# Kernel optimization log

Measured on AMD Instinct MI355X. Metric: run time of the kernel, lower is better.

The kernel has to match this reference:

```python
import math
import jax, jax.numpy as jnp
import numpy as np

B, LQ, LK = 4, 1024, 1024
D_MODEL, NHEAD, FFN = 1024, 16, 4096
DEPTH = D_MODEL // NHEAD  # 64
MAX_REL = 1024
EPS = 1e-5


def _rel_embedding():
    # fixed (non-learned) buffer: clamped relative-position indices used as float values
    length = max(MAX_REL, DEPTH)
    r = np.arange(length)
    mat = np.clip(r[None, :] - r[:, None], -MAX_REL, MAX_REL) + MAX_REL
    return jnp.asarray(mat[:MAX_REL, :DEPTH], jnp.float32)  # [MAX_REL, DEPTH]


def _skew(rel, length_k):
    # rel: [B, H, Lq, Lq] -> relative logits aligned to key positions [B, H, Lq, Lk]
    b, h, lq, m = rel.shape
    assert lq == m
    rel = jnp.pad(rel, ((0, 0), (0, 0), (0, 0), (1, 0)))
    rel = rel.reshape(b, h, lq + 1, lq)[:, :, 1:, :]
    if length_k > lq:
        rel = jnp.pad(rel, ((0, 0), (0, 0), (0, 0), (0, length_k - lq)))
    elif length_k < lq:
        rel = rel[:, :, :, :length_k]
    return rel


def _split_heads(t):
    b, l, _ = t.shape
    return t.reshape(b, l, NHEAD, DEPTH).transpose(0, 2, 1, 3)  # [b,h,l,d]


def _rga(x_q, x_kv, Wq, bq, Wo, bo, mask, rel_e):
    # NOTE: faithful to source - Q, K and V all use query_projection
    q = _split_heads(x_q @ Wq + bq)
    k = _split_heads(x_kv @ Wq + bq)
    v = _split_heads(x_kv @ Wq + bq)
    lq, lk = q.shape[2], k.shape[2]
    logits = jnp.einsum('bhqd,bhkd->bhqk', q, k)
    start = max(0, MAX_REL - lq)
    ke = rel_e[start:, :]  # [min(MAX_REL,lq), DEPTH]
    rel = jnp.einsum('bhld,md->bhlm', q, ke)
    logits = (logits + _skew(rel, lk)) / math.sqrt(DEPTH)
    if mask is not None:
        logits = jnp.where(mask, logits, jnp.asarray(-1e9, logits.dtype))
    w = jax.nn.softmax(logits, axis=-1)
    out = jnp.einsum('bhqk,bhkd->bhqd', w, v)
    out = out.transpose(0, 2, 1, 3).reshape(x_q.shape[0], lq, D_MODEL)
    return out @ Wo + bo


def _layernorm(x, g, b):
    mu = jnp.mean(x, axis=-1, keepdims=True)
    var = jnp.mean(jnp.square(x - mu), axis=-1, keepdims=True)
    return (x - mu) * jax.lax.rsqrt(var + EPS) * g + b


def setup_inputs() -> dict:
    key = jax.random.key(0)
    ks = jax.random.split(key, 12)
    s = 0.02
    inp = {
        'tgt': jax.random.normal(ks[0], (B, LQ, D_MODEL), jnp.float32),
        'memory': jax.random.normal(ks[1], (B, LK, D_MODEL), jnp.float32),
        'tgt_mask': jnp.tril(jnp.ones((LQ, LQ), dtype=bool)),
        'sa_Wq': jax.random.normal(ks[2], (D_MODEL, D_MODEL), jnp.float32) * s,
        'sa_bq': jnp.zeros((D_MODEL,), jnp.float32),
        'sa_Wo': jax.random.normal(ks[3], (D_MODEL, D_MODEL), jnp.float32) * s,
        'sa_bo': jnp.zeros((D_MODEL,), jnp.float32),
        'ca_Wq': jax.random.normal(ks[4], (D_MODEL, D_MODEL), jnp.float32) * s,
        'ca_bq': jnp.zeros((D_MODEL,), jnp.float32),
        'ca_Wo': jax.random.normal(ks[5], (D_MODEL, D_MODEL), jnp.float32) * s,
        'ca_bo': jnp.zeros((D_MODEL,), jnp.float32),
        'ffn_W1': jax.random.normal(ks[6], (D_MODEL, FFN), jnp.float32) * s,
        'ffn_b1': jnp.zeros((FFN,), jnp.float32),
        'ffn_W2': jax.random.normal(ks[7], (FFN, D_MODEL), jnp.float32) * s,
        'ffn_b2': jnp.zeros((D_MODEL,), jnp.float32),
        'ln1_g': jnp.ones((D_MODEL,), jnp.float32), 'ln1_b': jnp.zeros((D_MODEL,), jnp.float32),
        'ln2_g': jnp.ones((D_MODEL,), jnp.float32), 'ln2_b': jnp.zeros((D_MODEL,), jnp.float32),
        'ln3_g': jnp.ones((D_MODEL,), jnp.float32), 'ln3_b': jnp.zeros((D_MODEL,), jnp.float32),
    }
    return inp


def reference(tgt, memory, tgt_mask, sa_Wq, sa_bq, sa_Wo, sa_bo, ca_Wq, ca_bq, ca_Wo, ca_bo,
              ffn_W1, ffn_b1, ffn_W2, ffn_b2, ln1_g, ln1_b, ln2_g, ln2_b, ln3_g, ln3_b):
    rel_e = _rel_embedding()
    # self-attention (relative-global) with causal mask
    x = tgt + _rga(tgt, tgt, sa_Wq, sa_bq, sa_Wo, sa_bo, tgt_mask, rel_e)
    x = _layernorm(x, ln1_g, ln1_b)
    # cross-attention (also relative-global per source)
    x = x + _rga(x, memory, ca_Wq, ca_bq, ca_Wo, ca_bo, None, rel_e)
    x = _layernorm(x, ln2_g, ln2_b)
    # FFN
    h = jax.nn.relu(x @ ffn_W1 + ffn_b1)
    x = x + (h @ ffn_W2 + ffn_b2)
    x = _layernorm(x, ln3_g, ln3_b)
    return x
```

## Files before the change

### kernel.cpp

```cpp
#include <hip/hip_runtime.h>

typedef __attribute__((ext_vector_type(4))) float f32x4;
typedef __attribute__((ext_vector_type(8))) short s16x8;
typedef __attribute__((ext_vector_type(4))) unsigned short u16x4;

__device__ __forceinline__ unsigned short f2bf(float x) {
  union { float f; unsigned u; } un; un.f = x;
  unsigned u = un.u;
  u += 0x7FFFu + ((u >> 16) & 1u);
  return (unsigned short)(u >> 16);
}
__device__ __forceinline__ float bf2f(unsigned short h) {
  union { unsigned u; float f; } un; un.u = ((unsigned)h) << 16; return un.f;
}

__device__ __forceinline__ f32x4 mfma16(s16x8 a, s16x8 b, f32x4 c) {
  asm("v_mfma_f32_16x16x32_bf16 %0, %1, %2, %0" : "+v"(c) : "v"(a), "v"(b));
  return c;
}

__device__ __forceinline__ void gld16(const void* g, void* l) {
  __builtin_amdgcn_global_load_lds(
      (const __attribute__((address_space(1))) void*)g,
      (__attribute__((address_space(3))) void*)l, 16, 0, 0);
}

template<bool RELU, bool RESID, bool OUT_BF16>
__global__ __launch_bounds__(256, 2) void bgemm_k(
    const unsigned short* __restrict__ Ab, const unsigned short* __restrict__ Bb,
    const float* __restrict__ bias, const float* __restrict__ resid,
    void* __restrict__ Cp, int M, int N, int K, int lbx)
{
  __shared__ __align__(16) unsigned short As[2][128 * 64];
  __shared__ __align__(16) unsigned short Bs[2][128 * 64];

  const int nwg = gridDim.x;
  const int bid = blockIdx.x;
  const int swz = (bid & 7) * (nwg >> 3) + (bid >> 3);
  const int nbx_m1 = (1 << lbx) - 1;
  const int n0 = (swz & nbx_m1) * 128;
  const int m0 = (swz >> lbx) * 128;

  const int tid = threadIdx.x;
  const int lane = tid & 63;
  const int w = tid >> 6;
  const int wm = w >> 1, wn = w & 1;
  const int li = lane & 15, g = lane >> 4;

  f32x4 acc[4][4] = {};

#define STAGE(buf, kt) do { \
    const int k0_ = (kt) * 64; \
    _Pragma("unroll") \
    for (int i_ = 0; i_ < 4; i_++) { \
      int lin = i_ * 256 + tid; int row = lin >> 3; \
      int cg = (lin & 7) ^ (row & 7); \
      gld16(Ab + (size_t)(m0 + row) * K + k0_ + cg * 8, &As[buf][lin * 8]); \
    } \
    _Pragma("unroll") \
    for (int i_ = 0; i_ < 4; i_++) { \
      int lin = i_ * 256 + tid; int row = lin >> 3; \
      int cg = (lin & 7) ^ (row & 7); \
      gld16(Bb + (size_t)(n0 + row) * K + k0_ + cg * 8, &Bs[buf][lin * 8]); \
    } \
  } while (0)

  const int NT = K >> 6;
  STAGE(0, 0);
  for (int t = 0; t < NT; ++t) {
    const int cur = t & 1;
    if (t + 1 < NT) {
      STAGE(cur ^ 1, t + 1);
      asm volatile("s_waitcnt vmcnt(8)" ::: "memory");
    } else {
      asm volatile("s_waitcnt vmcnt(0)" ::: "memory");
    }
    __builtin_amdgcn_sched_barrier(0);
    __builtin_amdgcn_s_barrier();
    __builtin_amdgcn_sched_barrier(0);
#pragma unroll
    for (int ks = 0; ks < 2; ++ks) {
      s16x8 af[4], bf[4];
#pragma unroll
      for (int mt = 0; mt < 4; mt++) {
        int row = wm * 64 + mt * 16 + li;
        int slot = (4 * ks + g) ^ (row & 7);
        af[mt] = *(const s16x8*)&As[cur][row * 64 + slot * 8];
      }
#pragma unroll
      for (int nt = 0; nt < 4; nt++) {
        int row = wn * 64 + nt * 16 + li;
        int slot = (4 * ks + g) ^ (row & 7);
        bf[nt] = *(const s16x8*)&Bs[cur][row * 64 + slot * 8];
      }
#pragma unroll
      for (int mt = 0; mt < 4; mt++)
#pragma unroll
        for (int nt = 0; nt < 4; nt++)
          acc[mt][nt] = mfma16(af[mt], bf[nt], acc[mt][nt]);
    }
    __builtin_amdgcn_sched_barrier(0);
    __builtin_amdgcn_s_barrier();
    __builtin_amdgcn_sched_barrier(0);
  }
#undef STAGE

  asm volatile("s_nop 7\n\ts_nop 7" :::);
#pragma unroll
  for (int mt = 0; mt < 4; mt++) {
    int mrow = m0 + wm * 64 + mt * 16 + 4 * g;
#pragma unroll
    for (int nt = 0; nt < 4; nt++) {
      int ncol = n0 + wn * 64 + nt * 16 + li;
      float bv = bias ? bias[ncol] : 0.f;
#pragma unroll
      for (int r = 0; r < 4; r++) {
        int mr = mrow + r;
        float v = acc[mt][nt][r] + bv;
        if (RESID) v += resid[(size_t)mr * N + ncol];
        if (RELU) v = fmaxf(v, 0.f);
        if (OUT_BF16) ((unsigned short*)Cp)[(size_t)mr * N + ncol] = f2bf(v);
        else          ((float*)Cp)[(size_t)mr * N + ncol] = v;
      }
    }
  }
}

__global__ __launch_bounds__(256, 2) void bgemm_pk(
    const unsigned short* __restrict__ Ab, const unsigned short* __restrict__ Bb,
    float* __restrict__ P0, float* __restrict__ P1,
    int M, int N, int K, int KH, int lbx)
{
  __shared__ __align__(16) unsigned short As[2][128 * 64];
  __shared__ __align__(16) unsigned short Bs[2][128 * 64];

  const int nwg = gridDim.x;
  const int bid = blockIdx.x;
  const int swz = (bid & 7) * (nwg >> 3) + (bid >> 3);
  const int nbx_m1 = (1 << lbx) - 1;
  const int n0 = (swz & nbx_m1) * 128;
  int m0 = (swz >> lbx) * 128;

  int kb = 0;
  float* Pp = P0;
  if (m0 >= M) { m0 -= M; kb = KH; Pp = P1; }

  const int tid = threadIdx.x;
  const int lane = tid & 63;
  const int w = tid >> 6;
  const int wm = w >> 1, wn = w & 1;
  const int li = lane & 15, g = lane >> 4;

  f32x4 acc[4][4] = {};

#define PSTAGE(buf, kt) do { \
    const int k0_ = kb + (kt) * 64; \
    _Pragma("unroll") \
    for (int i_ = 0; i_ < 4; i_++) { \
      int lin = i_ * 256 + tid; int row = lin >> 3; \
      int cg = (lin & 7) ^ (row & 7); \
      gld16(Ab + (size_t)(m0 + row) * K + k0_ + cg * 8, &As[buf][lin * 8]); \
    } \
    _Pragma("unroll") \
    for (int i_ = 0; i_ < 4; i_++) { \
      int lin = i_ * 256 + tid; int row = lin >> 3; \
      int cg = (lin & 7) ^ (row & 7); \
      gld16(Bb + (size_t)(n0 + row) * K + k0_ + cg * 8, &Bs[buf][lin * 8]); \
    } \
  } while (0)

  const int NT = KH >> 6;
  PSTAGE(0, 0);
  for (int t = 0; t < NT; ++t) {
    const int cur = t & 1;
    if (t + 1 < NT) {
      PSTAGE(cur ^ 1, t + 1);
      asm volatile("s_waitcnt vmcnt(8)" ::: "memory");
    } else {
      asm volatile("s_waitcnt vmcnt(0)" ::: "memory");
    }
    __builtin_amdgcn_sched_barrier(0);
    __builtin_amdgcn_s_barrier();
    __builtin_amdgcn_sched_barrier(0);
#pragma unroll
    for (int ks = 0; ks < 2; ++ks) {
      s16x8 af[4], bf[4];
#pragma unroll
      for (int mt = 0; mt < 4; mt++) {
        int row = wm * 64 + mt * 16 + li;
        int slot = (4 * ks + g) ^ (row & 7);
        af[mt] = *(const s16x8*)&As[cur][row * 64 + slot * 8];
      }
#pragma unroll
      for (int nt = 0; nt < 4; nt++) {
        int row = wn * 64 + nt * 16 + li;
        int slot = (4 * ks + g) ^ (row & 7);
        bf[nt] = *(const s16x8*)&Bs[cur][row * 64 + slot * 8];
      }
#pragma unroll
      for (int mt = 0; mt < 4; mt++)
#pragma unroll
        for (int nt = 0; nt < 4; nt++)
          acc[mt][nt] = mfma16(af[mt], bf[nt], acc[mt][nt]);
    }
    __builtin_amdgcn_sched_barrier(0);
    __builtin_amdgcn_s_barrier();
    __builtin_amdgcn_sched_barrier(0);
  }
#undef PSTAGE

  asm volatile("s_nop 7\n\ts_nop 7" :::);
#pragma unroll
  for (int mt = 0; mt < 4; mt++) {
    int mrow = m0 + wm * 64 + mt * 16 + 4 * g;
#pragma unroll
    for (int nt = 0; nt < 4; nt++) {
      int ncol = n0 + wn * 64 + nt * 16 + li;
#pragma unroll
      for (int r = 0; r < 4; r++) {
        int mr = mrow + r;
        Pp[(size_t)mr * N + ncol] = acc[mt][nt][r];
      }
    }
  }
}

__global__ __launch_bounds__(256, 2) void sgemm_k(
    const unsigned short* __restrict__ Ah, const unsigned short* __restrict__ Al,
    const unsigned short* __restrict__ A2h, const unsigned short* __restrict__ A2l,
    const unsigned short* __restrict__ Bh, const unsigned short* __restrict__ Bl,
    const float* __restrict__ bias,
    unsigned short* __restrict__ Cb, unsigned short* __restrict__ C2b,
    int Ms, int M, int N, int K, int lbx)
{
  __shared__ __align__(16) unsigned short AsH[128 * 64];
  __shared__ __align__(16) unsigned short AsL[128 * 64];
  __shared__ __align__(16) unsigned short BsH[128 * 64];
  __shared__ __align__(16) unsigned short BsL[128 * 64];

  const int nwg = gridDim.x;
  const int bid = blockIdx.x;
  const int swz = (bid & 7) * (nwg >> 3) + (bid >> 3);
  const int nbx_m1 = (1 << lbx) - 1;
  const int n0 = (swz & nbx_m1) * 128;
  int m0 = (swz >> lbx) * 128;

  const unsigned short* Ahp = Ah;
  const unsigned short* Alp = Al;
  unsigned short* Cp = Cb;
  if (m0 >= Ms) { Ahp = A2h; Alp = A2l; Cp = C2b; m0 -= Ms; }

  const int tid = threadIdx.x;
  const int lane = tid & 63;
  const int w = tid >> 6;
  const int wm = w >> 1, wn = w & 1;
  const int li = lane & 15, g = lane >> 4;

  f32x4 acc[4][4] = {};

  const int NT = K >> 6;
  for (int t = 0; t < NT; ++t) {
    __syncthreads();
#pragma unroll
    for (int i = 0; i < 4; i++) {
      int lin = i * 256 + tid; int row = lin >> 3;
      int cg = (lin & 7) ^ (row & 7);
      size_t offA = (size_t)(m0 + row) * K + t * 64 + cg * 8;
      size_t offB = (size_t)(n0 + row) * K + t * 64 + cg * 8;
      gld16(Ahp + offA, &AsH[lin * 8]);
      gld16(Alp + offA, &AsL[lin * 8]);
      gld16(Bh + offB, &BsH[lin * 8]);
      gld16(Bl + offB, &BsL[lin * 8]);
    }
    asm volatile("s_waitcnt vmcnt(0)" ::: "memory");
    __syncthreads();
#pragma unroll
    for (int ks = 0; ks < 2; ++ks) {
      s16x8 ah[4], al[4], bh[4], bl[4];
#pragma unroll
      for (int mt = 0; mt < 4; mt++) {
        int row = wm * 64 + mt * 16 + li;
        int slot = (4 * ks + g) ^ (row & 7);
        ah[mt] = *(const s16x8*)&AsH[row * 64 + slot * 8];
        al[mt] = *(const s16x8*)&AsL[row * 64 + slot * 8];
      }
#pragma unroll
      for (int nt = 0; nt < 4; nt++) {
        int row = wn * 64 + nt * 16 + li;
        int slot = (4 * ks + g) ^ (row & 7);
        bh[nt] = *(const s16x8*)&BsH[row * 64 + slot * 8];
        bl[nt] = *(const s16x8*)&BsL[row * 64 + slot * 8];
      }
#pragma unroll
      for (int mt = 0; mt < 4; mt++)
#pragma unroll
        for (int nt = 0; nt < 4; nt++) {
          acc[mt][nt] = mfma16(ah[mt], bh[nt], acc[mt][nt]);
          acc[mt][nt] = mfma16(ah[mt], bl[nt], acc[mt][nt]);
          acc[mt][nt] = mfma16(al[mt], bh[nt], acc[mt][nt]);
        }
    }
  }

  asm volatile("s_nop 7\n\ts_nop 7" :::);
#pragma unroll
  for (int mt = 0; mt < 4; mt++) {
    int mrow = m0 + wm * 64 + mt * 16 + 4 * g;
#pragma unroll
    for (int nt = 0; nt < 4; nt++) {
      int ncol = n0 + wn * 64 + nt * 16 + li;
      float bv = bias[ncol];
#pragma unroll
      for (int r = 0; r < 4; r++) {
        int mr = mrow + r;
        Cp[(size_t)mr * N + ncol] = f2bf(acc[mt][nt][r] + bv);
      }
    }
  }
}

__device__ __forceinline__ void dev_tc(const float* __restrict__ W,
    unsigned short* __restrict__ WT, int K, int N, int bid, char* ldsu)
{
  unsigned short (*Ls)[65] = (unsigned short (*)[65])ldsu;
  int ntx = N >> 6;
  int ty = bid / ntx, tx = bid - ty * ntx;
  int r0 = ty << 6, c0 = tx << 6;
  int tid = threadIdx.x;
  int rl = tid >> 4, cl = (tid & 15) << 2;
#pragma unroll
  for (int rr = 0; rr < 4; rr++) {
    f32x4 v = *(const f32x4*)&W[(size_t)(r0 + rl + rr * 16) * N + c0 + cl];
#pragma unroll
    for (int j = 0; j < 4; j++) Ls[rl + rr * 16][cl + j] = f2bf(v[j]);
  }
  __syncthreads();
#pragma unroll
  for (int rr = 0; rr < 4; rr++) {
    int nl = rl + rr * 16;
    u16x4 o;
#pragma unroll
    for (int j = 0; j < 4; j++) o[j] = Ls[cl + j][nl];
    *(u16x4*)&WT[(size_t)(c0 + nl) * K + r0 + cl] = o;
  }
}

__device__ __forceinline__ void dev_tc2(const float* __restrict__ W,
    unsigned short* __restrict__ WTh, unsigned short* __restrict__ WTl,
    int K, int N, int bid, char* ldsu)
{
  float (*Ls)[65] = (float (*)[65])ldsu;
  int ntx = N >> 6;
  int ty = bid / ntx, tx = bid - ty * ntx;
  int r0 = ty << 6, c0 = tx << 6;
  int tid = threadIdx.x;
  int rl = tid >> 4, cl = (tid & 15) << 2;
#pragma unroll
  for (int rr = 0; rr < 4; rr++) {
    f32x4 v = *(const f32x4*)&W[(size_t)(r0 + rl + rr * 16) * N + c0 + cl];
#pragma unroll
    for (int j = 0; j < 4; j++) Ls[rl + rr * 16][cl + j] = v[j];
  }
  __syncthreads();
#pragma unroll
  for (int rr = 0; rr < 4; rr++) {
    int nl = rl + rr * 16;
    u16x4 oh, ol;
#pragma unroll
    for (int j = 0; j < 4; j++) {
      float v = Ls[cl + j][nl];
      unsigned short h = f2bf(v);
      oh[j] = h; ol[j] = f2bf(v - bf2f(h));
    }
    *(u16x4*)&WTh[(size_t)(c0 + nl) * K + r0 + cl] = oh;
    *(u16x4*)&WTl[(size_t)(c0 + nl) * K + r0 + cl] = ol;
  }
}

__global__ __launch_bounds__(256) void prep_w_k(
    const float* saWq, const float* caWq, const float* saWo, const float* caWo,
    const float* W1, const float* W2,
    unsigned short* WqTsaH, unsigned short* WqTsaL,
    unsigned short* WqTcaH, unsigned short* WqTcaL,
    unsigned short* WoTsa, unsigned short* WoTca,
    unsigned short* W1T, unsigned short* W2T)
{
  __shared__ __align__(16) char LDSU[64 * 65 * 4];
  int bid = blockIdx.x;
  if (bid < 256)       dev_tc2(saWq, WqTsaH, WqTsaL, 1024, 1024, bid, LDSU);
  else if (bid < 512)  dev_tc2(caWq, WqTcaH, WqTcaL, 1024, 1024, bid - 256, LDSU);
  else if (bid < 768)  dev_tc (saWo, WoTsa, 1024, 1024, bid - 512, LDSU);
  else if (bid < 1024) dev_tc (caWo, WoTca, 1024, 1024, bid - 768, LDSU);
  else if (bid < 2048) dev_tc (W1, W1T, 1024, 4096, bid - 1024, LDSU);
  else                 dev_tc (W2, W2T, 4096, 1024, bid - 2048, LDSU);
}

__device__ __forceinline__ void dev_cvt2row(const float* __restrict__ X,
    unsigned short* __restrict__ H, unsigned short* __restrict__ L, int bid)
{
  int i = (bid * 256 + threadIdx.x) * 4;
  f32x4 v = *(const f32x4*)&X[i];
  u16x4 hh, ll;
#pragma unroll
  for (int j = 0; j < 4; j++) {
    unsigned short h = f2bf(v[j]);
    hh[j] = h; ll[j] = f2bf(v[j] - bf2f(h));
  }
  *(u16x4*)&H[i] = hh;
  *(u16x4*)&L[i] = ll;
}

__device__ __forceinline__ void dev_wrel(const float* __restrict__ Wq,
    float* __restrict__ Wr, int bid)
{
  int idx = bid * 256 + threadIdx.x;
  int k = idx >> 4, h = idx & 15;
  const float* src = Wq + (size_t)k * 1024 + h * 64;
  float a = 0.f, s = 0.f;
#pragma unroll
  for (int d = 0; d < 64; d += 4) {
    f32x4 v = *(const f32x4*)&src[d];
#pragma unroll
    for (int j = 0; j < 4; j++) { a += v[j] * (float)(d + j + 1024); s += v[j]; }
  }
  Wr[k * 32 + h] = a;
  Wr[k * 32 + 16 + h] = s;
}

__device__ __forceinline__ void dev_crel(const float* __restrict__ bq,
    float* __restrict__ cr)
{
  int h = threadIdx.x;
  if (h < 16) {
    float a = 0.f, s = 0.f;
    for (int d = 0; d < 64; d++) { float v = bq[h * 64 + d]; a += v * (float)(d + 1024); s += v; }
    cr[h] = a; cr[16 + h] = s;
  }
}

__global__ __launch_bounds__(256) void prep_a_k(
    const float* tgt, const float* mem,
    unsigned short* tgth, unsigned short* tgtl,
    unsigned short* memh, unsigned short* meml,
    const float* saWq, const float* caWq, float* wrelsa, float* wrelca,
    const float* sabq, const float* cabq, float* crelsa, float* crelca)
{
  int bid = blockIdx.x;
  if (bid < 4096)       dev_cvt2row(tgt, tgth, tgtl, bid);
  else if (bid < 8192)  dev_cvt2row(mem, memh, meml, bid - 4096);
  else if (bid < 8256)  dev_wrel(saWq, wrelsa, bid - 8192);
  else if (bid < 8320)  dev_wrel(caWq, wrelca, bid - 8256);
  else if (bid == 8320) dev_crel(sabq, crelsa);
  else                  dev_crel(cabq, crelca);
}

__global__ __launch_bounds__(256) void relgemm_k(const float* __restrict__ X,
    const float* __restrict__ Wr, const float* __restrict__ cr,
    float* __restrict__ Out)
{
  __shared__ float Xs[8][256];
  __shared__ float Ws[256][32];
  int r0 = blockIdx.x * 8;
  int tid = threadIdx.x;
  int rl = tid >> 5, col = tid & 31;
  float acc = 0.f;
  for (int kc = 0; kc < 1024; kc += 256) {
    __syncthreads();
    {
      const float* xs = X + (size_t)(r0 + rl) * 1024 + kc + col * 8;
      *(f32x4*)&Xs[rl][col * 8] = *(const f32x4*)xs;
      *(f32x4*)&Xs[rl][col * 8 + 4] = *(const f32x4*)(xs + 4);
    }
    {
      const float* wsrc = Wr + (size_t)(kc + tid) * 32;
#pragma unroll
      for (int i = 0; i < 8; i++) *(f32x4*)&Ws[tid][i * 4] = *(const f32x4*)&wsrc[i * 4];
    }
    __syncthreads();
#pragma unroll 8
    for (int kk = 0; kk < 256; ++kk) acc += Xs[rl][kk] * Ws[kk][col];
  }
  Out[(size_t)(r0 + rl) * 32 + col] = acc + cr[col];
}

template<bool CAUSAL>
__global__ __launch_bounds__(512) void attn_k(
    const unsigned short* __restrict__ Qb, const unsigned short* __restrict__ KVb,
    const float* __restrict__ rAS, unsigned short* __restrict__ Ob)
{
  const int bh = blockIdx.x;
  const int b = bh >> 4, h = bh & 15;
  const int y = blockIdx.y;
  const int tid = threadIdx.x, lane = tid & 63, w = tid >> 6;
  const int g = lane >> 4, li = lane & 15;

  __shared__ __align__(16) unsigned short Kt[64 * 64];
  __shared__ __align__(16) unsigned short KT[64 * 64];
  __shared__ __align__(16) unsigned short Pl[8][16 * 64];

  const int tile = CAUSAL ? ((w < 4) ? y : (15 - y)) : (2 * y + (w >> 2));
  const int q0 = tile * 64 + (w & 3) * 16;
  const int nkb = CAUSAL ? (16 - y) : 16;

  s16x8 qf[2];
  {
    const unsigned short* qrow = Qb + (size_t)(b * 1024 + q0 + li) * 1024 + h * 64;
    qf[0] = *(const s16x8*)&qrow[8 * g];
    qf[1] = *(const s16x8*)&qrow[8 * g + 32];
  }
  const float SCL2 = 0.125f * 1.44269504f;
  int qri[4];
  float C0c[4], C1c[4], rSc[4], rS1c[4];
#pragma unroll
  for (int r = 0; r < 4; r++) {
    int qr = q0 + 4 * g + r;
    qri[r] = qr;
    float rA = rAS[(size_t)(b * 1024 + qr) * 32 + h];
    float rS = rAS[(size_t)(b * 1024 + qr) * 32 + 16 + h];
    int q1 = (qr + 1 < 1024) ? qr + 1 : 1023;
    float rA1 = rAS[(size_t)(b * 1024 + q1) * 32 + h];
    float rS1 = rAS[(size_t)(b * 1024 + q1) * 32 + 16 + h];
    C0c[r]  = (rA + (float)(qr - 1023) * rS) * SCL2;
    rSc[r]  = rS * SCL2;
    C1c[r]  = (rA1 + (float)(qr + 2) * rS1) * SCL2;
    rS1c[r] = rS1 * SCL2;
  }

  float mrow[4], lrow[4];
#pragma unroll
  for (int r = 0; r < 4; r++) { mrow[r] = -3.0e38f; lrow[r] = 0.f; }
  f32x4 accO[4] = {};

  for (int kbk = 0; kbk < nkb; kbk++) {
    __syncthreads();
    {
      const unsigned short* src = KVb + (size_t)(b * 1024 + kbk * 64 + lane) * 1024 + h * 64 + w * 8;
      s16x8 v = *(const s16x8*)src;
      int slot = w ^ (lane & 7);
      *(s16x8*)&Kt[lane * 64 + slot * 8] = v;
#pragma unroll
      for (int j = 0; j < 8; j++) {
        int d = w * 8 + j;
        KT[d * 64 + (((lane >> 3) ^ (d & 7)) * 8) + (lane & 7)] = (unsigned short)v[j];
      }
    }
    __syncthreads();
    if (!CAUSAL || kbk <= tile) {
      const bool diag = CAUSAL && (kbk == tile);
      f32x4 accS[4];
#pragma unroll
      for (int nt = 0; nt < 4; nt++) {
        int krow = li + 16 * nt;
        f32x4 c = {};
#pragma unroll
        for (int ks = 0; ks < 2; ks++) {
          int slot = (g + 4 * ks) ^ (krow & 7);
          s16x8 kf = *(const s16x8*)&Kt[krow * 64 + slot * 8];
          c = mfma16(qf[ks], kf, c);
        }
        accS[nt] = c;
      }
      float pv[4][4];
      float bm[4];
#pragma unroll
      for (int r = 0; r < 4; r++) bm[r] = -3.0e38f;
#pragma unroll
      for (int nt = 0; nt < 4; nt++) {
        int kk = kbk * 64 + 16 * nt + li;
        float kkf = (float)kk;
#pragma unroll
        for (int r = 0; r < 4; r++) {
          float sk = (kk <= qri[r]) ? fmaf(kkf, -rSc[r], C0c[r])
                   : ((kk == qri[r] + 1) ? 0.f : fmaf(kkf, -rS1c[r], C1c[r]));
          float lg = fmaf(accS[nt][r], SCL2, sk);
          if (diag && kk > qri[r]) lg = -1.0e9f;
          pv[nt][r] = lg;
          bm[r] = fmaxf(bm[r], lg);
        }
      }
#pragma unroll
      for (int off = 1; off < 16; off <<= 1)
#pragma unroll
        for (int r = 0; r < 4; r++)
          bm[r] = fmaxf(bm[r], __shfl_xor(bm[r], off, 64));
      float scl[4], rsum[4];
#pragma unroll
      for (int r = 0; r < 4; r++) {
        float mnew = fmaxf(mrow[r], bm[r]);
        scl[r] = exp2f(mrow[r] - mnew);
        mrow[r] = mnew;
        rsum[r] = 0.f;
      }
#pragma unroll
      for (int nt = 0; nt < 4; nt++)
#pragma unroll
        for (int r = 0; r < 4; r++) {
          float p = exp2f(pv[nt][r] - mrow[r]);
          pv[nt][r] = p;
          rsum[r] += p;
        }
#pragma unroll
      for (int off = 1; off < 16; off <<= 1)
#pragma unroll
        for (int r = 0; r < 4; r++)
          rsum[r] += __shfl_xor(rsum[r], off, 64);
#pragma unroll
      for (int r = 0; r < 4; r++) lrow[r] = lrow[r] * scl[r] + rsum[r];
#pragma unroll
      for (int nt = 0; nt < 4; nt++)
#pragma unroll
        for (int r = 0; r < 4; r++) {
          int qq = 4 * g + r;
          int kkk = 16 * nt + li;
          int slot = (kkk >> 3) ^ (qq & 7);
          Pl[w][qq * 64 + slot * 8 + (kkk & 7)] = f2bf(pv[nt][r]);
        }
#pragma unroll
      for (int dt = 0; dt < 4; dt++)
#pragma unroll
        for (int r = 0; r < 4; r++) accO[dt][r] *= scl[r];
      s16x8 pfk[2];
#pragma unroll
      for (int ks = 0; ks < 2; ks++) {
        int slotA = (g + 4 * ks) ^ (li & 7);
        pfk[ks] = *(const s16x8*)&Pl[w][li * 64 + slotA * 8];
      }
#pragma unroll
      for (int dt = 0; dt < 4; dt++) {
#pragma unroll
        for (int ks = 0; ks < 2; ks++) {
          int drow = li + 16 * dt;
          int slotB = (g + 4 * ks) ^ (drow & 7);
          s16x8 vf = *(const s16x8*)&KT[drow * 64 + slotB * 8];
          accO[dt] = mfma16(pfk[ks], vf, accO[dt]);
        }
      }
    }
  }
  asm volatile("s_nop 7\n\ts_nop 7" :::);
#pragma unroll
  for (int dt = 0; dt < 4; dt++) {
    int dcol = h * 64 + li + 16 * dt;
#pragma unroll
    for (int r = 0; r < 4; r++) {
      int q = q0 + 4 * g + r;
      Ob[(size_t)(b * 1024 + q) * 1024 + dcol] = f2bf(accO[dt][r] / lrow[r]);
    }
  }
}

__global__ __launch_bounds__(256) void redln_k(
    const float* __restrict__ P0, const float* __restrict__ P1,
    const float* __restrict__ bias, const float* __restrict__ resid,
    const float* __restrict__ gw, const float* __restrict__ bw,
    float* __restrict__ O, unsigned short* __restrict__ Obh,
    unsigned short* __restrict__ Obl)
{
  int row = blockIdx.x;
  int tid = threadIdx.x;
  size_t base = (size_t)row * 1024 + tid * 4;
  f32x4 a = *(const f32x4*)&P0[base];
  f32x4 b = *(const f32x4*)&P1[base];
  f32x4 c = *(const f32x4*)&resid[base];
  f32x4 bv = *(const f32x4*)&bias[tid * 4];
  f32x4 v;
#pragma unroll
  for (int j = 0; j < 4; j++) v[j] = a[j] + b[j] + bv[j] + c[j];
  float s = v[0] + v[1] + v[2] + v[3];
  float s2 = v[0]*v[0] + v[1]*v[1] + v[2]*v[2] + v[3]*v[3];
#pragma unroll
  for (int off = 32; off > 0; off >>= 1) {
    s += __shfl_down(s, off, 64);
    s2 += __shfl_down(s2, off, 64);
  }
  __shared__ float rb[8];
  if ((tid & 63) == 0) { rb[tid >> 6] = s; rb[4 + (tid >> 6)] = s2; }
  __syncthreads();
  float S = rb[0] + rb[1] + rb[2] + rb[3];
  float S2 = rb[4] + rb[5] + rb[6] + rb[7];
  float mu = S * (1.f / 1024.f);
  float var = S2 * (1.f / 1024.f) - mu * mu;
  float rstd = rsqrtf(var + 1e-5f);
  f32x4 go = *(const f32x4*)&gw[tid * 4];
  f32x4 bo = *(const f32x4*)&bw[tid * 4];
  f32x4 r;
#pragma unroll
  for (int j = 0; j < 4; j++) r[j] = (v[j] - mu) * rstd * go[j] + bo[j];
  *(f32x4*)&O[base] = r;
  if (Obh) {
    u16x4 oh;
#pragma unroll
    for (int j = 0; j < 4; j++) oh[j] = f2bf(r[j]);
    *(u16x4*)&Obh[base] = oh;
    if (Obl) {
      u16x4 ol;
#pragma unroll
      for (int j = 0; j < 4; j++) ol[j] = f2bf(r[j] - bf2f(f2bf(r[j])));
      *(u16x4*)&Obl[base] = ol;
    }
  }
}

extern "C" void kernel_launch(void* const* d_in, const int* in_sizes, int n_in,
                              void* d_out, int out_size, void* d_ws, size_t ws_size,
                              hipStream_t stream)
{
  const float* tgt  = (const float*)d_in[0];
  const float* mem  = (const float*)d_in[1];
  const float* saWq = (const float*)d_in[3];
  const float* sabq = (const float*)d_in[4];
  const float* saWo = (const float*)d_in[5];
  const float* sabo = (const float*)d_in[6];
  const float* caWq = (const float*)d_in[7];
  const float* cabq = (const float*)d_in[8];
  const float* caWo = (const float*)d_in[9];
  const float* cabo = (const float*)d_in[10];
  const float* W1   = (const float*)d_in[11];
  const float* b1   = (const float*)d_in[12];
  const float* W2   = (const float*)d_in[13];
  const float* b2   = (const float*)d_in[14];
  const float* g1   = (const float*)d_in[15];
  const float* be1  = (const float*)d_in[16];
  const float* g2   = (const float*)d_in[17];
  const float* be2  = (const float*)d_in[18];
  const float* g3   = (const float*)d_in[19];
  const float* be3  = (const float*)d_in[20];
  float* out = (float*)d_out;

  char* ws = (char*)d_ws;
  const size_t ACT = (size_t)4096 * 1024;
  unsigned short* RA   = (unsigned short*)ws; ws += ACT * 2;
  unsigned short* RB   = (unsigned short*)ws; ws += ACT * 2;
  unsigned short* qkvb = (unsigned short*)ws; ws += ACT * 2;
  unsigned short* kvb  = (unsigned short*)ws; ws += ACT * 2;
  unsigned short* x2b  = (unsigned short*)ws; ws += ACT * 2;
  unsigned short* RF   = (unsigned short*)ws; ws += (size_t)4096 * 4096 * 2;
  unsigned short* memh = RF;
  unsigned short* meml = RF + ACT;
  unsigned short* hb   = RF;
  float* Pq = (float*)qkvb;
  float* PR = (float*)RA;
  unsigned short* WqTsaH = (unsigned short*)ws; ws += (size_t)1024 * 1024 * 2;
  unsigned short* WqTsaL = (unsigned short*)ws; ws += (size_t)1024 * 1024 * 2;
  unsigned short* WoTsa  = (unsigned short*)ws; ws += (size_t)1024 * 1024 * 2;
  unsigned short* WqTcaH = (unsigned short*)ws; ws += (size_t)1024 * 1024 * 2;
  unsigned short* WqTcaL = (unsigned short*)ws; ws += (size_t)1024 * 1024 * 2;
  unsigned short* WoTca  = (unsigned short*)ws; ws += (size_t)1024 * 1024 * 2;
  unsigned short* W1T = (unsigned short*)ws; ws += (size_t)4096 * 1024 * 2;
  unsigned short* W2T = (unsigned short*)ws; ws += (size_t)4096 * 1024 * 2;
  float* x2f = (float*)ws; ws += (size_t)4096 * 1024 * 4;
  float* rAS = (float*)ws; ws += (size_t)4096 * 32 * 4;
  float* wrelsa = (float*)ws; ws += (size_t)1024 * 32 * 4;
  float* wrelca = (float*)ws; ws += (size_t)1024 * 32 * 4;
  float* crelsa = (float*)ws; ws += 128;
  float* crelca = (float*)ws; ws += 128;
  float* x1f = out;

  dim3 blk(256);

  prep_w_k<<<dim3(3072), blk, 0, stream>>>(saWq, caWq, saWo, caWo, W1, W2,
      WqTsaH, WqTsaL, WqTcaH, WqTcaL, WoTsa, WoTca, W1T, W2T);
  prep_a_k<<<dim3(8322), blk, 0, stream>>>(tgt, mem, RA, RB, memh, meml,
      saWq, caWq, wrelsa, wrelca, sabq, cabq, crelsa, crelca);

  sgemm_k<<<dim3(256), blk, 0, stream>>>(RA, RB, RA, RB, WqTsaH, WqTsaL, sabq,
      qkvb, qkvb, 1 << 30, 4096, 1024, 1024, 3);
  relgemm_k<<<dim3(512), blk, 0, stream>>>(tgt, wrelsa, crelsa, rAS);
  attn_k<true><<<dim3(64, 8), dim3(512), 0, stream>>>(qkvb, qkvb, rAS, RA);
  bgemm_pk<<<dim3(512), blk, 0, stream>>>(RA, WoTsa, x2f, Pq, 4096, 1024, 1024, 512, 3);
  redln_k<<<dim3(4096), blk, 0, stream>>>(x2f, Pq, sabo, tgt, g1, be1, x1f, RA, RB);
  sgemm_k<<<dim3(512), blk, 0, stream>>>(RA, RB, memh, meml, WqTcaH, WqTcaL, cabq,
      qkvb, kvb, 4096, 8192, 1024, 1024, 3);
  relgemm_k<<<dim3(512), blk, 0, stream>>>(x1f, wrelca, crelca, rAS);
  attn_k<false><<<dim3(64, 8), dim3(512), 0, stream>>>(qkvb, kvb, rAS, RA);
  bgemm_pk<<<dim3(512), blk, 0, stream>>>(RA, WoTca, x2f, Pq, 4096, 1024, 1024, 512, 3);
  redln_k<<<dim3(4096), blk, 0, stream>>>(x2f, Pq, cabo, x1f, g2, be2, x2f, x2b, nullptr);
  bgemm_k<true, false, true><<<dim3(1024), blk, 0, stream>>>(x2b, W1T, b1, nullptr, hb, 4096, 4096, 1024, 5);
  bgemm_pk<<<dim3(512), blk, 0, stream>>>(hb, W2T, Pq, PR, 4096, 1024, 4096, 2048, 3);
  redln_k<<<dim3(4096), blk, 0, stream>>>(Pq, PR, b2, x2f, g3, be3, out, nullptr, nullptr);

  (void)in_sizes; (void)n_in; (void)out_size; (void)ws_size;
}
```

Measured before the change: 453.4 us.

## Replace split-bf16 QKV projection GEMM with single fp16 MFMA double-buffered GEMM

The Q/K/V projection GEMMs previously emulated higher precision by splitting operands into hi/lo bf16 pairs and issuing three MFMAs per tile. They now convert activations and weights once to fp16 and issue a single fp16 MFMA, cutting both MFMA count and operand bandwidth to about a third. The new GEMM also double-buffers LDS tiles so the next K-slice loads overlap compute. Attention output is moved to a separate buffer so RA/RB can hold the fp16 inputs. The trade-off is lower precision for these projections and a risk of fp16 range overflow.

```diff
diff --git a/kernel.cpp b/kernel.cpp
--- a/kernel.cpp
+++ b/kernel.cpp
@@ -13,9 +13,16 @@
 __device__ __forceinline__ float bf2f(unsigned short h) {
   union { unsigned u; float f; } un; un.u = ((unsigned)h) << 16; return un.f;
 }
+__device__ __forceinline__ unsigned short f2h(float x) {
+  union { _Float16 h; unsigned short u; } un; un.h = (_Float16)x; return un.u;
+}
 
 __device__ __forceinline__ f32x4 mfma16(s16x8 a, s16x8 b, f32x4 c) {
   asm("v_mfma_f32_16x16x32_bf16 %0, %1, %2, %0" : "+v"(c) : "v"(a), "v"(b));
+  return c;
+}
+__device__ __forceinline__ f32x4 mfma16h(s16x8 a, s16x8 b, f32x4 c) {
+  asm("v_mfma_f32_16x16x32_f16 %0, %1, %2, %0" : "+v"(c) : "v"(a), "v"(b));
   return c;
 }
 
@@ -225,18 +232,14 @@
   }
 }
 
-__global__ __launch_bounds__(256, 2) void sgemm_k(
-    const unsigned short* __restrict__ Ah, const unsigned short* __restrict__ Al,
-    const unsigned short* __restrict__ A2h, const unsigned short* __restrict__ A2l,
-    const unsigned short* __restrict__ Bh, const unsigned short* __restrict__ Bl,
-    const float* __restrict__ bias,
+__global__ __launch_bounds__(256, 2) void hgemm_k(
+    const unsigned short* __restrict__ Af, const unsigned short* __restrict__ A2f,
+    const unsigned short* __restrict__ Bf, const float* __restrict__ bias,
     unsigned short* __restrict__ Cb, unsigned short* __restrict__ C2b,
     int Ms, int M, int N, int K, int lbx)
 {
-  __shared__ __align__(16) unsigned short AsH[128 * 64];
-  __shared__ __align__(16) unsigned short AsL[128 * 64];
-  __shared__ __align__(16) unsigned short BsH[128 * 64];
-  __shared__ __align__(16) unsigned short BsL[128 * 64];
+  __shared__ __align__(16) unsigned short As[2][128 * 64];
+  __shared__ __align__(16) unsigned short Bs[2][128 * 64];
 
   const int nwg = gridDim.x;
   const int bid = blockIdx.x;
@@ -245,10 +248,9 @@
   const int n0 = (swz & nbx_m1) * 128;
   int m0 = (swz >> lbx) * 128;
 
-  const unsigned short* Ahp = Ah;
-  const unsigned short* Alp = Al;
+  const unsigned short* Ap = Af;
   unsigned short* Cp = Cb;
-  if (m0 >= Ms) { Ahp = A2h; Alp = A2l; Cp = C2b; m0 -= Ms; }
+  if (m0 >= Ms) { Ap = A2f; Cp = C2b; m0 -= Ms; }
 
   const int tid = threadIdx.x;
   const int lane = tid & 63;
@@ -258,49 +260,61 @@
 
   f32x4 acc[4][4] = {};
 
+#define HSTAGE(buf, kt) do { \
+    const int k0_ = (kt) * 64; \
+    _Pragma("unroll") \
+    for (int i_ = 0; i_ < 4; i_++) { \
+      int lin = i_ * 256 + tid; int row = lin >> 3; \
+      int cg = (lin & 7) ^ (row & 7); \
+      gld16(Ap + (size_t)(m0 + row) * K + k0_ + cg * 8, &As[buf][lin * 8]); \
+    } \
+    _Pragma("unroll") \
+    for (int i_ = 0; i_ < 4; i_++) { \
+      int lin = i_ * 256 + tid; int row = lin >> 3; \
+      int cg = (lin & 7) ^ (row & 7); \
+      gld16(Bf + (size_t)(n0 + row) * K + k0_ + cg * 8, &Bs[buf][lin * 8]); \
+    } \
+  } while (0)
+
   const int NT = K >> 6;
+  HSTAGE(0, 0);
   for (int t = 0; t < NT; ++t) {
-    __syncthreads();
-#pragma unroll
-    for (int i = 0; i < 4; i++) {
-      int lin = i * 256 + tid; int row = lin >> 3;
-      int cg = (lin & 7) ^ (row & 7);
-      size_t offA = (size_t)(m0 + row) * K + t * 64 + cg * 8;
-      size_t offB = (size_t)(n0 + row) * K + t * 64 + cg * 8;
-      gld16(Ahp + offA, &AsH[lin * 8]);
-      gld16(Alp + offA, &AsL[lin * 8]);
-      gld16(Bh + offB, &BsH[lin * 8]);
-      gld16(Bl + offB, &BsL[lin * 8]);
-    }
-    asm volatile("s_waitcnt vmcnt(0)" ::: "memory");
-    __syncthreads();
+    const int cur = t & 1;
+    if (t + 1 < NT) {
+      HSTAGE(cur ^ 1, t + 1);
+      asm volatile("s_waitcnt vmcnt(8)" ::: "memory");
+    } else {
+      asm volatile("s_waitcnt vmcnt(0)" ::: "memory");
+    }
+    __builtin_amdgcn_sched_barrier(0);
+    __builtin_amdgcn_s_barrier();
+    __builtin_amdgcn_sched_barrier(0);
 #pragma unroll
     for (int ks = 0; ks < 2; ++ks) {
-      s16x8 ah[4], al[4], bh[4], bl[4];
+      s16x8 af[4], bf[4];
 #pragma unroll
       for (int mt = 0; mt < 4; mt++) {
         int row = wm * 64 + mt * 16 + li;
         int slot = (4 * ks + g) ^ (row & 7);
-        ah[mt] = *(const s16x8*)&AsH[row * 64 + slot * 8];
-        al[mt] = *(const s16x8*)&AsL[row * 64 + slot * 8];
+        af[mt] = *(const s16x8*)&As[cur][row * 64 + slot * 8];
       }
 #pragma unroll
       for (int nt = 0; nt < 4; nt++) {
         int row = wn * 64 + nt * 16 + li;
         int slot = (4 * ks + g) ^ (row & 7);
-        bh[nt] = *(const s16x8*)&BsH[row * 64 + slot * 8];
-        bl[nt] = *(const s16x8*)&BsL[row * 64 + slot * 8];
+        bf[nt] = *(const s16x8*)&Bs[cur][row * 64 + slot * 8];
       }
 #pragma unroll
       for (int mt = 0; mt < 4; mt++)
 #pragma unroll
-        for (int nt = 0; nt < 4; nt++) {
-          acc[mt][nt] = mfma16(ah[mt], bh[nt], acc[mt][nt]);
-          acc[mt][nt] = mfma16(ah[mt], bl[nt], acc[mt][nt]);
-          acc[mt][nt] = mfma16(al[mt], bh[nt], acc[mt][nt]);
-        }
-    }
-  }
+        for (int nt = 0; nt < 4; nt++)
+          acc[mt][nt] = mfma16h(af[mt], bf[nt], acc[mt][nt]);
+    }
+    __builtin_amdgcn_sched_barrier(0);
+    __builtin_amdgcn_s_barrier();
+    __builtin_amdgcn_sched_barrier(0);
+  }
+#undef HSTAGE
 
   asm volatile("s_nop 7\n\ts_nop 7" :::);
 #pragma unroll
@@ -345,11 +359,10 @@
   }
 }
 
-__device__ __forceinline__ void dev_tc2(const float* __restrict__ W,
-    unsigned short* __restrict__ WTh, unsigned short* __restrict__ WTl,
-    int K, int N, int bid, char* ldsu)
-{
-  float (*Ls)[65] = (float (*)[65])ldsu;
+__device__ __forceinline__ void dev_tcH(const float* __restrict__ W,
+    unsigned short* __restrict__ WT, int K, int N, int bid, char* ldsu)
+{
+  unsigned short (*Ls)[65] = (unsigned short (*)[65])ldsu;
   int ntx = N >> 6;
   int ty = bid / ntx, tx = bid - ty * ntx;
   int r0 = ty << 6, c0 = tx << 6;
@@ -359,55 +372,45 @@
   for (int rr = 0; rr < 4; rr++) {
     f32x4 v = *(const f32x4*)&W[(size_t)(r0 + rl + rr * 16) * N + c0 + cl];
 #pragma unroll
-    for (int j = 0; j < 4; j++) Ls[rl + rr * 16][cl + j] = v[j];
+    for (int j = 0; j < 4; j++) Ls[rl + rr * 16][cl + j] = f2h(v[j]);
   }
   __syncthreads();
 #pragma unroll
   for (int rr = 0; rr < 4; rr++) {
     int nl = rl + rr * 16;
-    u16x4 oh, ol;
-#pragma unroll
-    for (int j = 0; j < 4; j++) {
-      float v = Ls[cl + j][nl];
-      unsigned short h = f2bf(v);
-      oh[j] = h; ol[j] = f2bf(v - bf2f(h));
-    }
-    *(u16x4*)&WTh[(size_t)(c0 + nl) * K + r0 + cl] = oh;
-    *(u16x4*)&WTl[(size_t)(c0 + nl) * K + r0 + cl] = ol;
+    u16x4 o;
+#pragma unroll
+    for (int j = 0; j < 4; j++) o[j] = Ls[cl + j][nl];
+    *(u16x4*)&WT[(size_t)(c0 + nl) * K + r0 + cl] = o;
   }
 }
 
 __global__ __launch_bounds__(256) void prep_w_k(
     const float* saWq, const float* caWq, const float* saWo, const float* caWo,
     const float* W1, const float* W2,
-    unsigned short* WqTsaH, unsigned short* WqTsaL,
-    unsigned short* WqTcaH, unsigned short* WqTcaL,
+    unsigned short* WqTsaF, unsigned short* WqTcaF,
     unsigned short* WoTsa, unsigned short* WoTca,
     unsigned short* W1T, unsigned short* W2T)
 {
   __shared__ __align__(16) char LDSU[64 * 65 * 4];
   int bid = blockIdx.x;
-  if (bid < 256)       dev_tc2(saWq, WqTsaH, WqTsaL, 1024, 1024, bid, LDSU);
-  else if (bid < 512)  dev_tc2(caWq, WqTcaH, WqTcaL, 1024, 1024, bid - 256, LDSU);
+  if (bid < 256)       dev_tcH(saWq, WqTsaF, 1024, 1024, bid, LDSU);
+  else if (bid < 512)  dev_tcH(caWq, WqTcaF, 1024, 1024, bid - 256, LDSU);
   else if (bid < 768)  dev_tc (saWo, WoTsa, 1024, 1024, bid - 512, LDSU);
   else if (bid < 1024) dev_tc (caWo, WoTca, 1024, 1024, bid - 768, LDSU);
   else if (bid < 2048) dev_tc (W1, W1T, 1024, 4096, bid - 1024, LDSU);
   else                 dev_tc (W2, W2T, 4096, 1024, bid - 2048, LDSU);
 }
 
-__device__ __forceinline__ void dev_cvt2row(const float* __restrict__ X,
-    unsigned short* __restrict__ H, unsigned short* __restrict__ L, int bid)
+__device__ __forceinline__ void dev_cvtH(const float* __restrict__ X,
+    unsigned short* __restrict__ H, int bid)
 {
   int i = (bid * 256 + threadIdx.x) * 4;
   f32x4 v = *(const f32x4*)&X[i];
-  u16x4 hh, ll;
-#pragma unroll
-  for (int j = 0; j < 4; j++) {
-    unsigned short h = f2bf(v[j]);
-    hh[j] = h; ll[j] = f2bf(v[j] - bf2f(h));
-  }
+  u16x4 hh;
+#pragma unroll
+  for (int j = 0; j < 4; j++) hh[j] = f2h(v[j]);
   *(u16x4*)&H[i] = hh;
-  *(u16x4*)&L[i] = ll;
 }
 
 __device__ __forceinline__ void dev_wrel(const float* __restrict__ Wq,
@@ -440,14 +443,13 @@
 
 __global__ __launch_bounds__(256) void prep_a_k(
     const float* tgt, const float* mem,
-    unsigned short* tgth, unsigned short* tgtl,
-    unsigned short* memh, unsigned short* meml,
+    unsigned short* tgtf, unsigned short* memf,
     const float* saWq, const float* caWq, float* wrelsa, float* wrelca,
     const float* sabq, const float* cabq, float* crelsa, float* crelca)
 {
   int bid = blockIdx.x;
-  if (bid < 4096)       dev_cvt2row(tgt, tgth, tgtl, bid);
-  else if (bid < 8192)  dev_cvt2row(mem, memh, meml, bid - 4096);
+  if (bid < 4096)       dev_cvtH(tgt, tgtf, bid);
+  else if (bid < 8192)  dev_cvtH(mem, memf, bid - 4096);
   else if (bid < 8256)  dev_wrel(saWq, wrelsa, bid - 8192);
   else if (bid < 8320)  dev_wrel(caWq, wrelca, bid - 8256);
   else if (bid == 8320) dev_crel(sabq, crelsa);
@@ -649,12 +651,12 @@
   }
 }
 
+template<bool F16OUT>
 __global__ __launch_bounds__(256) void redln_k(
     const float* __restrict__ P0, const float* __restrict__ P1,
     const float* __restrict__ bias, const float* __restrict__ resid,
     const float* __restrict__ gw, const float* __restrict__ bw,
-    float* __restrict__ O, unsigned short* __restrict__ Obh,
-    unsigned short* __restrict__ Obl)
+    float* __restrict__ O, unsigned short* __restrict__ Obh)
 {
   int row = blockIdx.x;
   int tid = threadIdx.x;
@@ -690,14 +692,8 @@
   if (Obh) {
     u16x4 oh;
 #pragma unroll
-    for (int j = 0; j < 4; j++) oh[j] = f2bf(r[j]);
+    for (int j = 0; j < 4; j++) oh[j] = F16OUT ? f2h(r[j]) : f2bf(r[j]);
     *(u16x4*)&Obh[base] = oh;
-    if (Obl) {
-      u16x4 ol;
-#pragma unroll
-      for (int j = 0; j < 4; j++) ol[j] = f2bf(r[j] - bf2f(f2bf(r[j])));
-      *(u16x4*)&Obl[base] = ol;
-    }
   }
 }
 
@@ -735,16 +731,13 @@
   unsigned short* kvb  = (unsigned short*)ws; ws += ACT * 2;
   unsigned short* x2b  = (unsigned short*)ws; ws += ACT * 2;
   unsigned short* RF   = (unsigned short*)ws; ws += (size_t)4096 * 4096 * 2;
-  unsigned short* memh = RF;
-  unsigned short* meml = RF + ACT;
+  unsigned short* attb = RF;
   unsigned short* hb   = RF;
   float* Pq = (float*)qkvb;
   float* PR = (float*)RA;
-  unsigned short* WqTsaH = (unsigned short*)ws; ws += (size_t)1024 * 1024 * 2;
-  unsigned short* WqTsaL = (unsigned short*)ws; ws += (size_t)1024 * 1024 * 2;
+  unsigned short* WqTsaF = (unsigned short*)ws; ws += (size_t)1024 * 1024 * 2;
+  unsigned short* WqTcaF = (unsigned short*)ws; ws += (size_t)1024 * 1024 * 2;
   unsigned short* WoTsa  = (unsigned short*)ws; ws += (size_t)1024 * 1024 * 2;
-  unsigned short* WqTcaH = (unsigned short*)ws; ws += (size_t)1024 * 1024 * 2;
-  unsigned short* WqTcaL = (unsigned short*)ws; ws += (size_t)1024 * 1024 * 2;
   unsigned short* WoTca  = (unsigned short*)ws; ws += (size_t)1024 * 1024 * 2;
   unsigned short* W1T = (unsigned short*)ws; ws += (size_t)4096 * 1024 * 2;
   unsigned short* W2T = (unsigned short*)ws; ws += (size_t)4096 * 1024 * 2;
@@ -759,25 +752,25 @@
   dim3 blk(256);
 
   prep_w_k<<<dim3(3072), blk, 0, stream>>>(saWq, caWq, saWo, caWo, W1, W2,
-      WqTsaH, WqTsaL, WqTcaH, WqTcaL, WoTsa, WoTca, W1T, W2T);
-  prep_a_k<<<dim3(8322), blk, 0, stream>>>(tgt, mem, RA, RB, memh, meml,
+      WqTsaF, WqTcaF, WoTsa, WoTca, W1T, W2T);
+  prep_a_k<<<dim3(8322), blk, 0, stream>>>(tgt, mem, RA, RB,
       saWq, caWq, wrelsa, wrelca, sabq, cabq, crelsa, crelca);
 
-  sgemm_k<<<dim3(256), blk, 0, stream>>>(RA, RB, RA, RB, WqTsaH, WqTsaL, sabq,
+  hgemm_k<<<dim3(256), blk, 0, stream>>>(RA, RA, WqTsaF, sabq,
       qkvb, qkvb, 1 << 30, 4096, 1024, 1024, 3);
   relgemm_k<<<dim3(512), blk, 0, stream>>>(tgt, wrelsa, crelsa, rAS);
-  attn_k<true><<<dim3(64, 8), dim3(512), 0, stream>>>(qkvb, qkvb, rAS, RA);
-  bgemm_pk<<<dim3(512), blk, 0, stream>>>(RA, WoTsa, x2f, Pq, 4096, 1024, 1024, 512, 3);
-  redln_k<<<dim3(4096), blk, 0, stream>>>(x2f, Pq, sabo, tgt, g1, be1, x1f, RA, RB);
-  sgemm_k<<<dim3(512), blk, 0, stream>>>(RA, RB, memh, meml, WqTcaH, WqTcaL, cabq,
+  attn_k<true><<<dim3(64, 8), dim3(512), 0, stream>>>(qkvb, qkvb, rAS, attb);
+  bgemm_pk<<<dim3(512), blk, 0, stream>>>(attb, WoTsa, x2f, Pq, 4096, 1024, 1024, 512, 3);
+  redln_k<true><<<dim3(4096), blk, 0, stream>>>(x2f, Pq, sabo, tgt, g1, be1, x1f, RA);
+  hgemm_k<<<dim3(512), blk, 0, stream>>>(RA, RB, WqTcaF, cabq,
       qkvb, kvb, 4096, 8192, 1024, 1024, 3);
   relgemm_k<<<dim3(512), blk, 0, stream>>>(x1f, wrelca, crelca, rAS);
-  attn_k<false><<<dim3(64, 8), dim3(512), 0, stream>>>(qkvb, kvb, rAS, RA);
-  bgemm_pk<<<dim3(512), blk, 0, stream>>>(RA, WoTca, x2f, Pq, 4096, 1024, 1024, 512, 3);
-  redln_k<<<dim3(4096), blk, 0, stream>>>(x2f, Pq, cabo, x1f, g2, be2, x2f, x2b, nullptr);
+  attn_k<false><<<dim3(64, 8), dim3(512), 0, stream>>>(qkvb, kvb, rAS, attb);
+  bgemm_pk<<<dim3(512), blk, 0, stream>>>(attb, WoTca, x2f, Pq, 4096, 1024, 1024, 512, 3);
+  redln_k<false><<<dim3(4096), blk, 0, stream>>>(x2f, Pq, cabo, x1f, g2, be2, x2f, x2b);
   bgemm_k<true, false, true><<<dim3(1024), blk, 0, stream>>>(x2b, W1T, b1, nullptr, hb, 4096, 4096, 1024, 5);
   bgemm_pk<<<dim3(512), blk, 0, stream>>>(hb, W2T, Pq, PR, 4096, 1024, 4096, 2048, 3);
-  redln_k<<<dim3(4096), blk, 0, stream>>>(Pq, PR, b2, x2f, g3, be3, out, nullptr, nullptr);
+  redln_k<false><<<dim3(4096), blk, 0, stream>>>(Pq, PR, b2, x2f, g3, be3, out, nullptr);
 
   (void)in_sizes; (void)n_in; (void)out_size; (void)ws_size;
 }
```

After: 415.1 us. 1.09x faster.
